# Performance work log

Measured on AMD Instinct MI355X. Metric: run time of the kernel, lower is better.

The kernel has to match this reference:

```python
import jax, jax.numpy as jnp
import numpy as np

# Module hyper-parameters (match init_kwargs)
H = 8          # num_heads
F = 32         # attention_filters
HF = H * F     # 256, equals input channels C
RY, RX = 2, 2  # spatial_radius
PH, PW = 2 * RY + 1, 2 * RX + 1
S = PH * PW    # 25 neighbor offsets


def setup_inputs() -> dict:
    key = jax.random.key(0)
    ks = jax.random.split(key, 6)
    B, Y, X, C = 8, 128, 128, 256
    x = jax.random.normal(ks[0], (B, Y, X, C), dtype=jnp.float32)
    sc = 0.02
    Wq = jax.random.normal(ks[1], (C, HF), dtype=jnp.float32) * sc
    Wk = jax.random.normal(ks[2], (C, HF), dtype=jnp.float32) * sc
    Wv = jax.random.normal(ks[3], (C, HF), dtype=jnp.float32) * sc
    Wout = jax.random.normal(ks[4], (HF, C), dtype=jnp.float32) * sc
    pos_emb = jax.random.normal(ks[5], (S, HF), dtype=jnp.float32) * sc
    return {"x": x, "Wq": Wq, "Wk": Wk, "Wv": Wv, "Wout": Wout, "pos_emb": pos_emb}


def _centers(n, r):
    # clipped patch-center coordinate for each position
    c = jnp.arange(n)
    return jnp.clip(c, r, n - r - 1)


def reference(x, Wq, Wk, Wv, Wout, pos_emb):
    B, Y, X, C = x.shape
    dtype = x.dtype
    # 1x1 conv projections == channel matmuls
    Q = jnp.einsum('byxc,cf->byxf', x, Wq)
    K = jnp.einsum('byxc,cf->byxf', x, Wk)
    V = jnp.einsum('byxc,cf->byxf', x, Wv)

    # query spatial positional embedding (relative position to clipped center)
    yc = _centers(Y, RY)
    xc = _centers(X, RX)
    y_rel = jnp.arange(Y) - yc + RY          # [Y]
    x_rel = jnp.arange(X) - xc + RX          # [X]
    q_idx = y_rel[:, None] * PW + x_rel[None, :]  # [Y, X]
    Q = Q + pos_emb[q_idx]                   # [B,Y,X,HF]
    Q = Q.reshape(B, Y, X, H, F)

    scale = jnp.asarray(1.0 / np.sqrt(F), dtype)

    offsets = [(dy, dx) for dy in range(-RY, RY + 1) for dx in range(-RX, RX + 1)]

    # pass 1: per-offset scores (loop over fixed 25-neighborhood, rest vectorized)
    scores = []
    for s_idx, (dy, dx) in enumerate(offsets):
        ny = jnp.clip(yc + dy, 0, Y - 1)     # [Y]
        nx = jnp.clip(xc + dx, 0, X - 1)     # [X]
        Kn = K[:, ny][:, :, nx] + pos_emb[s_idx]        # [B,Y,X,HF]
        Kn = Kn.reshape(B, Y, X, H, F)
        scores.append(jnp.einsum('byxhf,byxhf->byxh', Q, Kn) * scale)
    scores = jnp.stack(scores, axis=-1)      # [B,Y,X,H,S]
    weights = jax.nn.softmax(scores, axis=-1)

    # pass 2: weighted value accumulation
    out_acc = jnp.zeros((B, Y, X, H, F), dtype=dtype)
    for s_idx, (dy, dx) in enumerate(offsets):
        ny = jnp.clip(yc + dy, 0, Y - 1)
        nx = jnp.clip(xc + dx, 0, X - 1)
        Vn = V[:, ny][:, :, nx].reshape(B, Y, X, H, F)
        out_acc = out_acc + weights[..., s_idx, None] * Vn

    out_acc = out_acc.reshape(B, Y, X, HF)
    out = jnp.einsum('byxf,fc->byxc', out_acc, Wout)
    return out
```

## Files before the change

kernel.cpp:

```cpp
#include <hip/hip_runtime.h>
#include <hip/hip_fp16.h>

#define DEVI __device__ __forceinline__

typedef short v8s __attribute__((ext_vector_type(8)));
typedef float v4f __attribute__((ext_vector_type(4)));
typedef _Float16 h2v __attribute__((ext_vector_type(2)));
typedef __fp16 fp16x2 __attribute__((ext_vector_type(2)));
typedef unsigned short u16;

typedef __attribute__((address_space(3))) unsigned int lds_u32;
typedef const __attribute__((address_space(1))) unsigned int glb_u32;

DEVI float bf2f(short s) {
  union { unsigned u; float f; } cv;
  cv.u = ((unsigned)(u16)s) << 16;
  return cv.f;
}
DEVI short f2bf(float f) {
  union { float f; unsigned u; } cv; cv.f = f;
  unsigned u = cv.u;
  return (short)((u + 0x7FFFu + ((u >> 16) & 1u)) >> 16);
}
DEVI unsigned cvtpk(float lo, float hi) {
  unsigned r;
  asm("v_cvt_pk_bf16_f32 %0, %1, %2" : "=v"(r) : "v"(lo), "v"(hi));
  return r;
}
DEVI unsigned pkh(float a, float b) {
  union { fp16x2 h; unsigned u; } cv;
  cv.h = __builtin_amdgcn_cvt_pkrtz(a, b);
  return cv.u;
}
DEVI float fdot2u(unsigned a, unsigned b, float c) {
  union { unsigned u; h2v h; } ca, cb; ca.u = a; cb.u = b;
  return __builtin_amdgcn_fdot2(ca.h, cb.h, c, false);
}
DEVI __half2 uh2(unsigned u) { union { unsigned u; __half2 h; } c; c.u = u; return c.h; }
DEVI void gld16(const void* g, void* l) {
  __builtin_amdgcn_global_load_lds((glb_u32*)g, (lds_u32*)l, 16, 0, 0);
}
DEVI float pairsum(float part) {
  int o = __builtin_amdgcn_update_dpp(0, __float_as_int(part), 0xB1, 0xf, 0xf, true);
  return part + __int_as_float(o);
}

__global__ void prep_weights(const float* __restrict__ Wq, const float* __restrict__ Wk,
                             const float* __restrict__ Wv, const float* __restrict__ Wout,
                             short* __restrict__ WcT, short* __restrict__ WoT) {
  int n = blockIdx.x;
  int k = threadIdx.x;
  float v;
  if (n < 256)      v = Wq[k * 256 + n];
  else if (n < 512) v = Wk[k * 256 + (n - 256)];
  else              v = Wv[k * 256 + (n - 512)];
  WcT[n * 256 + k] = f2bf(v);
  if (n < 256) WoT[n * 256 + k] = f2bf(Wout[k * 256 + n]);
}

__global__ void x_cast(const float* __restrict__ x, short* __restrict__ xb) {
  for (size_t gidx = (size_t)blockIdx.x * 256 + threadIdx.x; gidx < 4194304;
       gidx += (size_t)4096 * 256) {
    const float4* src = reinterpret_cast<const float4*>(x + gidx * 8);
    float4 a = src[0], c = src[1];
    v8s pk;
    pk[0] = f2bf(a.x); pk[1] = f2bf(a.y); pk[2] = f2bf(a.z); pk[3] = f2bf(a.w);
    pk[4] = f2bf(c.x); pk[5] = f2bf(c.y); pk[6] = f2bf(c.z); pk[7] = f2bf(c.w);
    *reinterpret_cast<v8s*>(xb + gidx * 8) = pk;
  }
}

__launch_bounds__(512, 2)
__global__ void proj_gemm(const short* __restrict__ xb, const short* __restrict__ WcT,
                          const float* __restrict__ pos_emb,
                          short* __restrict__ Qb, short* __restrict__ Kb,
                          short* __restrict__ Vb) {
  __shared__ short As[2][256 * 64];
  __shared__ short Bs[2][256 * 64];
  const int t = threadIdx.x;
  const int bi = blockIdx.x;
  const int xcd = bi & 7;
  const int j = bi >> 3;
  const int mtl = j / 3, nt = j % 3;
  const int mt = xcd * 64 + mtl;
  const int m0 = mt * 256, n0 = nt * 256;
  const int wave = t >> 6, lane = t & 63;
  const int wm = (wave >> 2) * 128, wn = (wave & 3) * 64;
  const int lr = lane & 15, g = lane >> 4;

  const int ro = lane >> 3;
  const int colb = ((lane & 7) * 16) ^ (ro << 4);
  const char* aSrc0 = reinterpret_cast<const char*>(xb + (size_t)(m0 + ro) * 256) + colb;
  const char* bSrc0 = reinterpret_cast<const char*>(WcT + (size_t)(n0 + ro) * 256) + colb;

  auto stage = [&](int buf, int ks) {
#pragma unroll
    for (int c = 0; c < 4; ++c) {
      int cc = wave * 4 + c;
      gld16(aSrc0 + (size_t)cc * 8 * 512 + ks * 128, (char*)As[buf] + cc * 1024);
      gld16(bSrc0 + (size_t)cc * 8 * 512 + ks * 128, (char*)Bs[buf] + cc * 1024);
    }
  };

  v4f acc[8][4];
#pragma unroll
  for (int i = 0; i < 8; ++i)
#pragma unroll
    for (int jj = 0; jj < 4; ++jj) acc[i][jj] = (v4f){0.f, 0.f, 0.f, 0.f};

  stage(0, 0);
  __syncthreads();

#pragma unroll 1
  for (int s = 0; s < 4; ++s) {
    const int buf = s & 1;
    if (s < 3) stage(buf ^ 1, s + 1);

    const char* aB = (const char*)As[buf];
    const char* bB = (const char*)Bs[buf];
#pragma unroll
    for (int kk = 0; kk < 2; ++kk) {
      v8s bfr[4];
#pragma unroll
      for (int jj = 0; jj < 4; ++jj) {
        int rn = wn + jj * 16 + lr;
        bfr[jj] = *reinterpret_cast<const v8s*>(
            bB + ((rn * 128 + kk * 64 + g * 16) ^ ((rn & 7) << 4)));
      }
#pragma unroll
      for (int i = 0; i < 8; ++i) {
        int row = wm + i * 16 + lr;
        v8s af = *reinterpret_cast<const v8s*>(
            aB + ((row * 128 + kk * 64 + g * 16) ^ ((row & 7) << 4)));
#pragma unroll
        for (int jj = 0; jj < 4; ++jj)
          acc[i][jj] = __builtin_amdgcn_mfma_f32_16x16x32_bf16(bfr[jj], af, acc[i][jj], 0, 0, 0);
      }
    }
    __syncthreads();
  }

  short* dst = (nt == 0) ? Qb : (nt == 1) ? Kb : Vb;
#pragma unroll
  for (int i = 0; i < 8; ++i) {
    int p = m0 + wm + i * 16 + lr;
    int qi = 0;
    if (nt == 0) {
      int yy = (p >> 7) & 127, xx = p & 127;
      qi = (yy - min(max(yy, 2), 125) + 2) * 5 + (xx - min(max(xx, 2), 125) + 2);
    }
#pragma unroll
    for (int jj = 0; jj < 4; ++jj) {
      int nb = wn + jj * 16 + g * 4;
      v4f a = acc[i][jj];
      if (nt == 0) {
        float4 pe4 = *reinterpret_cast<const float4*>(pos_emb + qi * 256 + nb);
        a[0] += pe4.x; a[1] += pe4.y; a[2] += pe4.z; a[3] += pe4.w;
      }
      uint2 pk;
      pk.x = pkh(a[0], a[1]);
      pk.y = pkh(a[2], a[3]);
      *reinterpret_cast<uint2*>(dst + (size_t)p * 256 + nb) = pk;
    }
  }
}

__launch_bounds__(256, 4)
__global__ void attn_kernel(const short* __restrict__ Qb, const short* __restrict__ Kb,
                            const short* __restrict__ Vb, const float* __restrict__ pos_emb,
                            short* __restrict__ ACC) {
  __shared__ unsigned pe16[25 * 128];
  for (int i = threadIdx.x; i < 1600; i += 256) {
    float4 vv = reinterpret_cast<const float4*>(pos_emb)[i];
    int s = i >> 6;
    int jw = (i & 63) * 2;
    int e = ((jw >> 5) & 3) << 1;
    uint2 pk2;
    pk2.x = pkh(vv.x, vv.y);
    pk2.y = pkh(vv.z, vv.w);
    *reinterpret_cast<uint2*>(pe16 + s * 128 + (jw ^ e)) = pk2;
  }

  const int t = threadIdx.x;
  const int half = t & 1, h = (t >> 1) & 7, pl = t >> 4;
  const int id = blockIdx.x;
  const int b = id & 7;
  const int local = id >> 3;
  const int bx = local & 31, by = local >> 5;
  const int xx = bx * 4 + (pl & 3);
  const int yy = by * 4 + (pl >> 2);
  const int yc = min(max(yy, 2), 125), xc = min(max(xx, 2), 125);
  const int fo = h * 32 + half * 16;
  const size_t pbase = ((size_t)((b * 128 + yy) * 128 + xx)) * 256 + fo;
  const size_t cbase = ((size_t)((b * 128 + yc) * 128 + xc)) * 256 + fo;
  const float SCALE2 = 0.17677669529663689f * 1.4426950408889634f;

  uint4 qA = *reinterpret_cast<const uint4*>(Qb + pbase);
  uint4 qB = *reinterpret_cast<const uint4*>(Qb + pbase + 8);
  __syncthreads();

  float l = 0.f;
  __half2 oa[8];
#pragma unroll
  for (int jv = 0; jv < 8; ++jv) oa[jv] = uh2(0u);

  const short* kb = Kb + cbase;
  const short* vb = Vb + cbase;
  const int sw = h * 16 + half * 8;
  const int e = (h >> 1) << 1;

  uint4 k0a, k1a, v0a, v1a, k0b, k1b, v0b, v1b;
  {
    const short* kp = kb + (-2 * 128 - 2) * 256;
    const short* vp = vb + (-2 * 128 - 2) * 256;
    k0a = *reinterpret_cast<const uint4*>(kp);
    k1a = *reinterpret_cast<const uint4*>(kp + 8);
    v0a = *reinterpret_cast<const uint4*>(vp);
    v1a = *reinterpret_cast<const uint4*>(vp + 8);
    const short* kp1 = kb + (-2 * 128 - 1) * 256;
    const short* vp1 = vb + (-2 * 128 - 1) * 256;
    k0b = *reinterpret_cast<const uint4*>(kp1);
    k1b = *reinterpret_cast<const uint4*>(kp1 + 8);
    v0b = *reinterpret_cast<const uint4*>(vp1);
    v1b = *reinterpret_cast<const uint4*>(vp1 + 8);
  }

#pragma unroll 1
  for (int dy = -2; dy <= 2; ++dy) {
    const unsigned* prow = pe16 + ((dy + 2) * 5) * 128 + sw;
#pragma unroll
    for (int dxi = 0; dxi < 5; ++dxi) {
      const int dx = dxi - 2;
      uint4 k0 = k0a, k1 = k1a, v0 = v0a, v1 = v1a;
      k0a = k0b; k1a = k1b; v0a = v0b; v1a = v1b;
      int ndx = dx + 2, ndy = dy;
      if (ndx > 2) { ndx -= 5; ndy += 1; }
      if (ndy <= 2) {
        const short* kp2 = kb + (ndy * 128 + ndx) * 256;
        const short* vp2 = vb + (ndy * 128 + ndx) * 256;
        k0b = *reinterpret_cast<const uint4*>(kp2);
        k1b = *reinterpret_cast<const uint4*>(kp2 + 8);
        v0b = *reinterpret_cast<const uint4*>(vp2);
        v1b = *reinterpret_cast<const uint4*>(vp2 + 8);
      }
      const unsigned* ps = prow + dxi * 128;
      uint2 pp0 = *reinterpret_cast<const uint2*>(ps + (0 ^ e));
      uint2 pp1 = *reinterpret_cast<const uint2*>(ps + (2 ^ e));
      uint2 pp2 = *reinterpret_cast<const uint2*>(ps + (4 ^ e));
      uint2 pp3 = *reinterpret_cast<const uint2*>(ps + (6 ^ e));

      float d0 = 0.f, d1 = 0.f, d2 = 0.f, d3 = 0.f;
      d0 = fdot2u(qA.x, k0.x, d0); d1 = fdot2u(qA.y, k0.y, d1);
      d2 = fdot2u(qA.z, k0.z, d2); d3 = fdot2u(qA.w, k0.w, d3);
      d0 = fdot2u(qB.x, k1.x, d0); d1 = fdot2u(qB.y, k1.y, d1);
      d2 = fdot2u(qB.z, k1.z, d2); d3 = fdot2u(qB.w, k1.w, d3);
      d0 = fdot2u(qA.x, pp0.x, d0); d1 = fdot2u(qA.y, pp0.y, d1);
      d2 = fdot2u(qA.z, pp1.x, d2); d3 = fdot2u(qA.w, pp1.y, d3);
      d0 = fdot2u(qB.x, pp2.x, d0); d1 = fdot2u(qB.y, pp2.y, d1);
      d2 = fdot2u(qB.z, pp3.x, d2); d3 = fdot2u(qB.w, pp3.y, d3);

      float part = ((d0 + d1) + (d2 + d3)) * SCALE2;
      float full = pairsum(part);
      float w = exp2f(full);
      l += w;
      __half2 w2 = uh2(pkh(w, w));
      oa[0] = __hfma2(w2, uh2(v0.x), oa[0]);
      oa[1] = __hfma2(w2, uh2(v0.y), oa[1]);
      oa[2] = __hfma2(w2, uh2(v0.z), oa[2]);
      oa[3] = __hfma2(w2, uh2(v0.w), oa[3]);
      oa[4] = __hfma2(w2, uh2(v1.x), oa[4]);
      oa[5] = __hfma2(w2, uh2(v1.y), oa[5]);
      oa[6] = __hfma2(w2, uh2(v1.z), oa[6]);
      oa[7] = __hfma2(w2, uh2(v1.w), oa[7]);
    }
  }

  float inv = 1.f / l;
  uint4 s0, s1;
  s0.x = cvtpk(__low2float(oa[0]) * inv, __high2float(oa[0]) * inv);
  s0.y = cvtpk(__low2float(oa[1]) * inv, __high2float(oa[1]) * inv);
  s0.z = cvtpk(__low2float(oa[2]) * inv, __high2float(oa[2]) * inv);
  s0.w = cvtpk(__low2float(oa[3]) * inv, __high2float(oa[3]) * inv);
  s1.x = cvtpk(__low2float(oa[4]) * inv, __high2float(oa[4]) * inv);
  s1.y = cvtpk(__low2float(oa[5]) * inv, __high2float(oa[5]) * inv);
  s1.z = cvtpk(__low2float(oa[6]) * inv, __high2float(oa[6]) * inv);
  s1.w = cvtpk(__low2float(oa[7]) * inv, __high2float(oa[7]) * inv);
  *reinterpret_cast<uint4*>(ACC + pbase) = s0;
  *reinterpret_cast<uint4*>(ACC + pbase + 8) = s1;
}

__launch_bounds__(512, 2)
__global__ void out_gemm(const short* __restrict__ A, const short* __restrict__ WoT,
                         float* __restrict__ out) {
  __shared__ short As[2][256 * 64];
  __shared__ short Bs[2][256 * 64];
  const int t = threadIdx.x;
  const int bi = blockIdx.x;
  const int xcd = bi & 7;
  const int mt = xcd * 64 + (bi >> 3);
  const int m0 = mt * 256;
  const int wave = t >> 6, lane = t & 63;
  const int wm = (wave >> 2) * 128, wn = (wave & 3) * 64;
  const int lr = lane & 15, g = lane >> 4;

  const int ro = lane >> 3;
  const int colb = ((lane & 7) * 16) ^ (ro << 4);
  const char* aSrc0 = reinterpret_cast<const char*>(A + (size_t)(m0 + ro) * 256) + colb;
  const char* bSrc0 = reinterpret_cast<const char*>(WoT + (size_t)ro * 256) + colb;

  auto stage = [&](int buf, int ks) {
#pragma unroll
    for (int c = 0; c < 4; ++c) {
      int cc = wave * 4 + c;
      gld16(aSrc0 + (size_t)cc * 8 * 512 + ks * 128, (char*)As[buf] + cc * 1024);
      gld16(bSrc0 + (size_t)cc * 8 * 512 + ks * 128, (char*)Bs[buf] + cc * 1024);
    }
  };

  v4f acc[8][4];
#pragma unroll
  for (int i = 0; i < 8; ++i)
#pragma unroll
    for (int jj = 0; jj < 4; ++jj) acc[i][jj] = (v4f){0.f, 0.f, 0.f, 0.f};

  stage(0, 0);
  __syncthreads();

#pragma unroll 1
  for (int s = 0; s < 4; ++s) {
    const int buf = s & 1;
    if (s < 3) stage(buf ^ 1, s + 1);

    const char* aB = (const char*)As[buf];
    const char* bB = (const char*)Bs[buf];
#pragma unroll
    for (int kk = 0; kk < 2; ++kk) {
      v8s bfr[4];
#pragma unroll
      for (int jj = 0; jj < 4; ++jj) {
        int rn = wn + jj * 16 + lr;
        bfr[jj] = *reinterpret_cast<const v8s*>(
            bB + ((rn * 128 + kk * 64 + g * 16) ^ ((rn & 7) << 4)));
      }
#pragma unroll
      for (int i = 0; i < 8; ++i) {
        int row = wm + i * 16 + lr;
        v8s af = *reinterpret_cast<const v8s*>(
            aB + ((row * 128 + kk * 64 + g * 16) ^ ((row & 7) << 4)));
#pragma unroll
        for (int jj = 0; jj < 4; ++jj)
          acc[i][jj] = __builtin_amdgcn_mfma_f32_16x16x32_bf16(bfr[jj], af, acc[i][jj], 0, 0, 0);
      }
    }
    __syncthreads();
  }

#pragma unroll
  for (int i = 0; i < 8; ++i) {
    int p = m0 + wm + i * 16 + lr;
#pragma unroll
    for (int jj = 0; jj < 4; ++jj) {
      int nb = wn + jj * 16 + g * 4;
      float4 o;
      o.x = acc[i][jj][0]; o.y = acc[i][jj][1];
      o.z = acc[i][jj][2]; o.w = acc[i][jj][3];
      *reinterpret_cast<float4*>(out + (size_t)p * 256 + nb) = o;
    }
  }
}

extern "C" void kernel_launch(void* const* d_in, const int* in_sizes, int n_in,
                              void* d_out, int out_size, void* d_ws, size_t ws_size,
                              hipStream_t stream) {
  const float* x       = (const float*)d_in[0];
  const float* Wq      = (const float*)d_in[1];
  const float* Wk      = (const float*)d_in[2];
  const float* Wv      = (const float*)d_in[3];
  const float* Wout    = (const float*)d_in[4];
  const float* pos_emb = (const float*)d_in[5];
  float* out = (float*)d_out;

  char* ws = (char*)d_ws;
  short* WcT  = (short*)ws;
  short* WoT  = (short*)(ws + 393216);
  short* Qb   = (short*)(ws + 524288);
  short* Kb   = Qb + (size_t)131072 * 256;
  short* Vb   = Kb + (size_t)131072 * 256;
  short* ACCb = Vb + (size_t)131072 * 256;
  short* xb   = ACCb;

  prep_weights<<<768, 256, 0, stream>>>(Wq, Wk, Wv, Wout, WcT, WoT);
  x_cast<<<4096, 256, 0, stream>>>(x, xb);
  proj_gemm<<<1536, 512, 0, stream>>>(xb, WcT, pos_emb, Qb, Kb, Vb);
  attn_kernel<<<8192, 256, 0, stream>>>(Qb, Kb, Vb, pos_emb, ACCb);
  out_gemm<<<512, 512, 0, stream>>>(ACCb, WoT, out);
}
```

Measured before the change: 322.4 us.

## Fuse fp32-to-bf16 cast of x into projection GEMM A-tile staging

Removes the separate x_cast kernel and has proj_gemm read fp32 x directly, converting to bf16 in registers and writing swizzled tiles to LDS. The A loads for the next stage are split into two halves, interleaved with the two MFMA k-substeps so the global latency is hidden. This avoids writing and re-reading a 64 MB bf16 copy of x and one kernel launch. In exchange, each of the three N-tile blocks re-reads fp32 x (twice the bytes of bf16), and A staging now goes through registers instead of direct-to-LDS loads, which raises register pressure.

```diff
diff --git a/kernel.cpp b/kernel.cpp
--- a/kernel.cpp
+++ b/kernel.cpp
@@ -58,20 +58,8 @@
   if (n < 256) WoT[n * 256 + k] = f2bf(Wout[k * 256 + n]);
 }
 
-__global__ void x_cast(const float* __restrict__ x, short* __restrict__ xb) {
-  for (size_t gidx = (size_t)blockIdx.x * 256 + threadIdx.x; gidx < 4194304;
-       gidx += (size_t)4096 * 256) {
-    const float4* src = reinterpret_cast<const float4*>(x + gidx * 8);
-    float4 a = src[0], c = src[1];
-    v8s pk;
-    pk[0] = f2bf(a.x); pk[1] = f2bf(a.y); pk[2] = f2bf(a.z); pk[3] = f2bf(a.w);
-    pk[4] = f2bf(c.x); pk[5] = f2bf(c.y); pk[6] = f2bf(c.z); pk[7] = f2bf(c.w);
-    *reinterpret_cast<v8s*>(xb + gidx * 8) = pk;
-  }
-}
-
 __launch_bounds__(512, 2)
-__global__ void proj_gemm(const short* __restrict__ xb, const short* __restrict__ WcT,
+__global__ void proj_gemm(const float* __restrict__ x, const short* __restrict__ WcT,
                           const float* __restrict__ pos_emb,
                           short* __restrict__ Qb, short* __restrict__ Kb,
                           short* __restrict__ Vb) {
@@ -88,16 +76,36 @@
   const int wm = (wave >> 2) * 128, wn = (wave & 3) * 64;
   const int lr = lane & 15, g = lane >> 4;
 
+  const int r = t >> 1, kh = t & 1;
+  const float* aSrcF = x + (size_t)(m0 + r) * 256 + kh * 32;
+
   const int ro = lane >> 3;
   const int colb = ((lane & 7) * 16) ^ (ro << 4);
-  const char* aSrc0 = reinterpret_cast<const char*>(xb + (size_t)(m0 + ro) * 256) + colb;
   const char* bSrc0 = reinterpret_cast<const char*>(WcT + (size_t)(n0 + ro) * 256) + colb;
 
-  auto stage = [&](int buf, int ks) {
+  float4 fa[4];
+  auto ldA = [&](int s, int gg) {
+    const float* src = aSrcF + s * 64 + gg * 16;
+#pragma unroll
+    for (int j2 = 0; j2 < 4; ++j2) fa[j2] = *reinterpret_cast<const float4*>(src + j2 * 4);
+  };
+  auto wrA = [&](int buf, int gg) {
+#pragma unroll
+    for (int p = 0; p < 2; ++p) {
+      uint4 w;
+      w.x = cvtpk(fa[2 * p].x, fa[2 * p].y);
+      w.y = cvtpk(fa[2 * p].z, fa[2 * p].w);
+      w.z = cvtpk(fa[2 * p + 1].x, fa[2 * p + 1].y);
+      w.w = cvtpk(fa[2 * p + 1].z, fa[2 * p + 1].w);
+      int q = gg * 2 + p;
+      int byte = (r * 128 + kh * 64 + q * 16) ^ ((r & 7) << 4);
+      *reinterpret_cast<uint4*>((char*)As[buf] + byte) = w;
+    }
+  };
+  auto stB = [&](int buf, int ks) {
 #pragma unroll
     for (int c = 0; c < 4; ++c) {
       int cc = wave * 4 + c;
-      gld16(aSrc0 + (size_t)cc * 8 * 512 + ks * 128, (char*)As[buf] + cc * 1024);
       gld16(bSrc0 + (size_t)cc * 8 * 512 + ks * 128, (char*)Bs[buf] + cc * 1024);
     }
   };
@@ -108,35 +116,51 @@
 #pragma unroll
     for (int jj = 0; jj < 4; ++jj) acc[i][jj] = (v4f){0.f, 0.f, 0.f, 0.f};
 
-  stage(0, 0);
+  ldA(0, 0); wrA(0, 0); ldA(0, 1); wrA(0, 1);
+  stB(0, 0);
   __syncthreads();
 
 #pragma unroll 1
   for (int s = 0; s < 4; ++s) {
     const int buf = s & 1;
-    if (s < 3) stage(buf ^ 1, s + 1);
+    if (s < 3) { stB(buf ^ 1, s + 1); ldA(s + 1, 0); }
 
     const char* aB = (const char*)As[buf];
     const char* bB = (const char*)Bs[buf];
-#pragma unroll
-    for (int kk = 0; kk < 2; ++kk) {
+    {
       v8s bfr[4];
 #pragma unroll
       for (int jj = 0; jj < 4; ++jj) {
         int rn = wn + jj * 16 + lr;
-        bfr[jj] = *reinterpret_cast<const v8s*>(
-            bB + ((rn * 128 + kk * 64 + g * 16) ^ ((rn & 7) << 4)));
+        bfr[jj] = *reinterpret_cast<const v8s*>(bB + ((rn * 128 + g * 16) ^ ((rn & 7) << 4)));
       }
 #pragma unroll
       for (int i = 0; i < 8; ++i) {
         int row = wm + i * 16 + lr;
-        v8s af = *reinterpret_cast<const v8s*>(
-            aB + ((row * 128 + kk * 64 + g * 16) ^ ((row & 7) << 4)));
+        v8s af = *reinterpret_cast<const v8s*>(aB + ((row * 128 + g * 16) ^ ((row & 7) << 4)));
 #pragma unroll
         for (int jj = 0; jj < 4; ++jj)
           acc[i][jj] = __builtin_amdgcn_mfma_f32_16x16x32_bf16(bfr[jj], af, acc[i][jj], 0, 0, 0);
       }
     }
+    if (s < 3) { wrA(buf ^ 1, 0); ldA(s + 1, 1); }
+    {
+      v8s bfr[4];
+#pragma unroll
+      for (int jj = 0; jj < 4; ++jj) {
+        int rn = wn + jj * 16 + lr;
+        bfr[jj] = *reinterpret_cast<const v8s*>(bB + ((rn * 128 + 64 + g * 16) ^ ((rn & 7) << 4)));
+      }
+#pragma unroll
+      for (int i = 0; i < 8; ++i) {
+        int row = wm + i * 16 + lr;
+        v8s af = *reinterpret_cast<const v8s*>(aB + ((row * 128 + 64 + g * 16) ^ ((row & 7) << 4)));
+#pragma unroll
+        for (int jj = 0; jj < 4; ++jj)
+          acc[i][jj] = __builtin_amdgcn_mfma_f32_16x16x32_bf16(bfr[jj], af, acc[i][jj], 0, 0, 0);
+      }
+    }
+    if (s < 3) wrA(buf ^ 1, 1);
     __syncthreads();
   }
 
@@ -387,11 +411,9 @@
   short* Kb   = Qb + (size_t)131072 * 256;
   short* Vb   = Kb + (size_t)131072 * 256;
   short* ACCb = Vb + (size_t)131072 * 256;
-  short* xb   = ACCb;
 
   prep_weights<<<768, 256, 0, stream>>>(Wq, Wk, Wv, Wout, WcT, WoT);
-  x_cast<<<4096, 256, 0, stream>>>(x, xb);
-  proj_gemm<<<1536, 512, 0, stream>>>(xb, WcT, pos_emb, Qb, Kb, Vb);
+  proj_gemm<<<1536, 512, 0, stream>>>(x, WcT, pos_emb, Qb, Kb, Vb);
   attn_kernel<<<8192, 256, 0, stream>>>(Qb, Kb, Vb, pos_emb, ACCb);
   out_gemm<<<512, 512, 0, stream>>>(ACCb, WoT, out);
 }
```

New measurement: 365.5 us. 1.13x slower.
